# Kernel optimization log

Measured on AMD Instinct MI355X. Metric: run time of the kernel, lower is better.

## Reference

```python
import jax, jax.numpy as jnp
import numpy as np

N_NODES = 50000
N_EDGES = 625000
IN_CH = 128
OUT_CH = 128


def setup_inputs() -> dict:
    key = jax.random.key(0)
    k1, k2, k3, k4 = jax.random.split(key, 4)
    x = jax.random.normal(k1, (N_NODES, IN_CH), dtype=jnp.float32)
    edge_index = jax.random.randint(k2, (2, N_EDGES), 0, N_NODES, dtype=jnp.int64)
    # nn.Linear(in, out): weight [out, in], bias [out]
    bound = 1.0 / np.sqrt(IN_CH)
    W = jax.random.uniform(k3, (OUT_CH, IN_CH), minval=-bound, maxval=bound, dtype=jnp.float32)
    b = jax.random.uniform(k4, (OUT_CH,), minval=-bound, maxval=bound, dtype=jnp.float32)
    return {"x": x, "edge_index": edge_index, "W": W, "b": b}


def reference(x, edge_index, W, b):
    row, col = edge_index[0], edge_index[1]
    num_nodes = x.shape[0]
    # degree of destination nodes (scatter_add of ones over row)
    deg = jax.ops.segment_sum(jnp.ones(row.shape[0], dtype=x.dtype), row,
                              num_segments=num_nodes)
    deg_inv_sqrt = jnp.where(deg > 0, jax.lax.rsqrt(jnp.maximum(deg, 1.0)) * jnp.where(deg > 0, 1.0, 0.0), 0.0)
    deg_inv_sqrt = jnp.where(deg > 0, deg ** -0.5, 0.0)
    norm = deg_inv_sqrt[row] * deg_inv_sqrt[col]  # [E]
    src = x[col] * norm[:, None]                  # gather + scale, [E, C]
    out = jax.ops.segment_sum(src, row, num_segments=num_nodes)  # scatter-add
    return out @ W.T + b
```

## Files before the change

### kernel.cpp

```cpp
#include <hip/hip_runtime.h>
#include <hip/hip_bf16.h>

#define NN 50000
#define NE 625000
#define CH 128
#define RSTR 32
#define NG 196
#define GCAP 4096
#define NBIN 256
#define EPB 2442

typedef __attribute__((ext_vector_type(8))) short short8;
typedef __attribute__((ext_vector_type(4))) float floatx4;

__device__ __forceinline__ ushort f2bf(float v) {
    __hip_bfloat16 h = __float2bfloat16(v);
    return *(ushort*)&h;
}
__device__ __forceinline__ float bf2f(uint u) {
    return __uint_as_float(u << 16);
}

__global__ __launch_bounds__(256) void k_prep(const float* __restrict__ x,
                                              ushort* __restrict__ xb,
                                              const float* __restrict__ W,
                                              ushort* __restrict__ whi,
                                              ushort* __restrict__ wlo,
                                              const int* __restrict__ row,
                                              const int* __restrict__ col,
                                              uint* __restrict__ gbase,
                                              uint* __restrict__ gseg) {
    __shared__ uint h[NG];
    __shared__ uint sc[NG];
    __shared__ uint gb[NG];
    __shared__ uint cur[NG];
    __shared__ uint ss[256];
    __shared__ uint pk[EPB];

    int b = blockIdx.x;
    int t = threadIdx.x;
    if (b < NBIN) {
        int e0 = b * EPB;
        int n = NE - e0; if (n > EPB) n = EPB;

        for (int i = t; i < NG; i += 256) h[i] = 0;
        __syncthreads();

        int r[10], c[10];
#pragma unroll
        for (int j = 0; j < 10; ++j) {
            int i = t + j * 256;
            int idx = (i < n) ? (e0 + i) : e0;
            r[j] = row[idx];
            c[j] = col[idx];
        }
#pragma unroll
        for (int j = 0; j < 10; ++j)
            if (t + j * 256 < n) atomicAdd(&h[r[j] >> 8], 1u);
        __syncthreads();

        ss[t] = (t < NG) ? h[t] : 0u;
        __syncthreads();
        for (int off = 1; off < 256; off <<= 1) {
            uint add = (t >= off) ? ss[t - off] : 0u;
            __syncthreads();
            ss[t] += add;
            __syncthreads();
        }
        if (t < NG) {
            uint ex = (t == 0) ? 0u : ss[t - 1];
            sc[t] = ex;
            cur[t] = ex;
            if (h[t] > 0) gb[t] = atomicAdd(&gbase[t], h[t]);
        }
        __syncthreads();

#pragma unroll
        for (int j = 0; j < 10; ++j) {
            if (t + j * 256 < n) {
                int g = r[j] >> 8;
                uint p = atomicAdd(&cur[g], 1u);
                pk[p] = ((uint)(r[j] & 255) << 16) | (uint)(c[j] & 0xffff);
            }
        }
        __syncthreads();

        for (int i = t; i < n; i += 256) {
            int lo = 0, hi = NG - 1;
            while (lo < hi) {
                int mid = (lo + hi + 1) >> 1;
                if (sc[mid] <= (uint)i) lo = mid; else hi = mid - 1;
            }
            int g = lo;
            uint off = gb[g] + ((uint)i - sc[g]);
            if (off < GCAP) gseg[(size_t)g * GCAP + off] = pk[i];
        }
    } else if (b < 6506) {
        int i = ((b - 256) * 256 + t) * 4;
        float4 v = *(const float4*)(x + i);
        ushort4 o;
        o.x = f2bf(v.x); o.y = f2bf(v.y); o.z = f2bf(v.z); o.w = f2bf(v.w);
        *(ushort4*)(xb + i) = o;
    } else {
        int i = (b - 6506) * 256 + t;
        float v = W[i];
        ushort hh = f2bf(v);
        whi[i] = hh;
        wlo[i] = f2bf(v - bf2f((uint)hh));
    }
}

__global__ __launch_bounds__(256) void k_csr(const uint* __restrict__ gseg,
                                             const uint* __restrict__ gcnt,
                                             uint* __restrict__ csr,
                                             int* __restrict__ deg_c,
                                             float* __restrict__ nrm) {
    __shared__ ushort slots[64][62];
    __shared__ uint dcnt[64];
    int g = blockIdx.x >> 2;
    int q = blockIdx.x & 3;
    int t = threadIdx.x;

    int n = (int)gcnt[g];
    if (n > GCAP) n = GCAP;
    if (t < 64) dcnt[t] = 0;
    __syncthreads();

    const uint* seg = gseg + (size_t)g * GCAP;
    for (int i = t; i < n; i += 256) {
        uint p = seg[i];
        int rl = (int)(p >> 16);
        if ((rl >> 6) == q) {
            int r6 = rl & 63;
            uint k = atomicAdd(&dcnt[r6], 1u);
            if (k < 62) slots[r6][k] = (ushort)(p & 0xffff);
        }
    }
    __syncthreads();

    int row0 = g * 256 + q * 64;
    for (int i = t; i < 2048; i += 256) {
        int rl = i >> 5, w = i & 31;
        int rr = row0 + rl;
        if (rr < NN) {
            uint val;
            if (w == 0) val = dcnt[rl];
            else val = (uint)slots[rl][2 * w - 2] | ((uint)slots[rl][2 * w - 1] << 16);
            csr[(size_t)rr * RSTR + w] = val;
        }
    }
    if (t < 64) {
        int rr = row0 + t;
        if (rr < NN) {
            int d = (int)dcnt[t];
            deg_c[rr] = d;
            nrm[rr] = (d > 0) ? rsqrtf((float)d) : 0.0f;
        }
    }
}

__global__ __launch_bounds__(256) void k_agg(const ushort* __restrict__ xb,
                                             const int* __restrict__ deg_c,
                                             const float* __restrict__ nrm,
                                             const uint* __restrict__ csr,
                                             ushort* __restrict__ ahi) {
    const int wave = threadIdx.x >> 6;
    const int lane = threadIdx.x & 63;
    const int node = blockIdx.x * 4 + wave;
    const int deg = deg_c[node];
    const float dr = nrm[node];

    const ushort* slots = (const ushort*)(csr + node * RSTR) + 2;
    int li = (lane < 62) ? lane : 0;
    ushort craw = slots[li];
    int cli = (lane < deg) ? (int)craw : 0;
    float nl = (lane < deg) ? nrm[cli] : 0.0f;

    float ax = 0.0f, ay = 0.0f;
    for (int j = 0; j < deg; j += 8) {
#pragma unroll
        for (int u = 0; u < 8; ++u) {
            int cc = __shfl(cli, j + u);
            float nn = __shfl(nl, j + u);
            ushort2 v = ((const ushort2*)(xb + (size_t)cc * CH))[lane];
            ax = fmaf(bf2f((uint)v.x), nn, ax);
            ay = fmaf(bf2f((uint)v.y), nn, ay);
        }
    }

    ushort2 hv;
    hv.x = f2bf(ax * dr);
    hv.y = f2bf(ay * dr);
    ((ushort2*)(ahi + (size_t)node * CH))[lane] = hv;
}

__global__ __launch_bounds__(256) void k_mfma(const ushort* __restrict__ ahi,
                                              const ushort* __restrict__ whi,
                                              const ushort* __restrict__ wlo,
                                              const float* __restrict__ bias,
                                              float* __restrict__ out) {
    const int wave = threadIdx.x >> 6;
    const int lane = threadIdx.x & 63;
    const int quad = lane >> 4;
    const int r16 = lane & 15;
    const int m0 = blockIdx.x * 32;
    const int nt0 = wave * 2, nt1 = nt0 + 1;

    const ushort* a0p  = ahi + (size_t)(m0 + r16) * CH + quad * 8;
    const ushort* a1p  = a0p + 16 * CH;
    const ushort* bh0p = whi + (size_t)(nt0 * 16 + r16) * CH + quad * 8;
    const ushort* bl0p = wlo + (size_t)(nt0 * 16 + r16) * CH + quad * 8;
    const ushort* bh1p = whi + (size_t)(nt1 * 16 + r16) * CH + quad * 8;
    const ushort* bl1p = wlo + (size_t)(nt1 * 16 + r16) * CH + quad * 8;

    float b0 = bias[nt0 * 16 + r16];
    float b1 = bias[nt1 * 16 + r16];
    floatx4 acc00 = {b0, b0, b0, b0};
    floatx4 acc01 = {b1, b1, b1, b1};
    floatx4 acc10 = {b0, b0, b0, b0};
    floatx4 acc11 = {b1, b1, b1, b1};

#pragma unroll
    for (int kb = 0; kb < 4; ++kb) {
        const int k0 = kb * 32;
        short8 a0 = *(const short8*)(a0p + k0);
        short8 a1 = *(const short8*)(a1p + k0);
        short8 h0 = *(const short8*)(bh0p + k0);
        short8 l0 = *(const short8*)(bl0p + k0);
        short8 h1 = *(const short8*)(bh1p + k0);
        short8 l1 = *(const short8*)(bl1p + k0);
        acc00 = __builtin_amdgcn_mfma_f32_16x16x32_bf16(a0, h0, acc00, 0, 0, 0);
        acc00 = __builtin_amdgcn_mfma_f32_16x16x32_bf16(a0, l0, acc00, 0, 0, 0);
        acc01 = __builtin_amdgcn_mfma_f32_16x16x32_bf16(a0, h1, acc01, 0, 0, 0);
        acc01 = __builtin_amdgcn_mfma_f32_16x16x32_bf16(a0, l1, acc01, 0, 0, 0);
        acc10 = __builtin_amdgcn_mfma_f32_16x16x32_bf16(a1, h0, acc10, 0, 0, 0);
        acc10 = __builtin_amdgcn_mfma_f32_16x16x32_bf16(a1, l0, acc10, 0, 0, 0);
        acc11 = __builtin_amdgcn_mfma_f32_16x16x32_bf16(a1, h1, acc11, 0, 0, 0);
        acc11 = __builtin_amdgcn_mfma_f32_16x16x32_bf16(a1, l1, acc11, 0, 0, 0);
    }

#pragma unroll
    for (int r = 0; r < 4; ++r) {
        int row0 = m0 + quad * 4 + r;
        int row1 = row0 + 16;
        if (row0 < NN) {
            out[(size_t)row0 * CH + nt0 * 16 + r16] = acc00[r];
            out[(size_t)row0 * CH + nt1 * 16 + r16] = acc01[r];
        }
        if (row1 < NN) {
            out[(size_t)row1 * CH + nt0 * 16 + r16] = acc10[r];
            out[(size_t)row1 * CH + nt1 * 16 + r16] = acc11[r];
        }
    }
}

extern "C" void kernel_launch(void* const* d_in, const int* in_sizes, int n_in,
                              void* d_out, int out_size, void* d_ws, size_t ws_size,
                              hipStream_t stream) {
    const float* x = (const float*)d_in[0];
    const int* ei = (const int*)d_in[1];
    const float* W = (const float*)d_in[2];
    const float* b = (const float*)d_in[3];
    float* out = (float*)d_out;

    uint* csr = (uint*)d_ws;
    int* deg_c = (int*)(csr + (size_t)NN * RSTR);
    float* nrm = (float*)(deg_c + 50176);
    ushort* ahi = (ushort*)(nrm + 50176);
    ushort* xb = ahi + (size_t)(NN + 16) * CH;
    ushort* whi = xb + (size_t)NN * CH;
    ushort* wlo = whi + CH * CH;
    uint* gbase = (uint*)(wlo + CH * CH);
    uint* gseg = gbase + 256;

    hipMemsetAsync(gbase, 0, NG * sizeof(uint), stream);
    k_prep<<<6570, 256, 0, stream>>>(x, xb, W, whi, wlo, ei, ei + NE, gbase, gseg);
    k_csr<<<NG * 4, 256, 0, stream>>>(gseg, gbase, csr, deg_c, nrm);
    k_agg<<<NN / 4, 256, 0, stream>>>(xb, deg_c, nrm, csr, ahi);
    k_mfma<<<(NN + 31) / 32, 256, 0, stream>>>(ahi, whi, wlo, b, out);
}
```

Baseline: 145.5 us.

## Fuse neighbor aggregation into MFMA GEMM kernel via swizzled LDS tile

Merges the aggregation and linear-transform kernels into one. Each block aggregates 32 nodes (8 per wave) into a swizzled bf16 LDS tile and then runs the MFMA GEMM from LDS, so the intermediate aggregated matrix no longer makes a global-memory round trip and one launch is dropped. The gather now has each half-wave fetch a different neighbor with 8-byte loads, combined by a cross-half shuffle. Next-node metadata is prefetched while the current node is processed. The cost is fewer, heavier blocks (one per 32 nodes instead of one per 4), which may reduce latency hiding in the gather phase.

```diff
diff --git a/kernel.cpp b/kernel.cpp
--- a/kernel.cpp
+++ b/kernel.cpp
@@ -159,55 +159,82 @@
     }
 }
 
-__global__ __launch_bounds__(256) void k_agg(const ushort* __restrict__ xb,
-                                             const int* __restrict__ deg_c,
-                                             const float* __restrict__ nrm,
-                                             const uint* __restrict__ csr,
-                                             ushort* __restrict__ ahi) {
-    const int wave = threadIdx.x >> 6;
-    const int lane = threadIdx.x & 63;
-    const int node = blockIdx.x * 4 + wave;
-    const int deg = deg_c[node];
-    const float dr = nrm[node];
-
-    const ushort* slots = (const ushort*)(csr + node * RSTR) + 2;
-    int li = (lane < 62) ? lane : 0;
-    ushort craw = slots[li];
-    int cli = (lane < deg) ? (int)craw : 0;
-    float nl = (lane < deg) ? nrm[cli] : 0.0f;
-
-    float ax = 0.0f, ay = 0.0f;
-    for (int j = 0; j < deg; j += 8) {
-#pragma unroll
-        for (int u = 0; u < 8; ++u) {
-            int cc = __shfl(cli, j + u);
-            float nn = __shfl(nl, j + u);
-            ushort2 v = ((const ushort2*)(xb + (size_t)cc * CH))[lane];
-            ax = fmaf(bf2f((uint)v.x), nn, ax);
-            ay = fmaf(bf2f((uint)v.y), nn, ay);
-        }
-    }
-
-    ushort2 hv;
-    hv.x = f2bf(ax * dr);
-    hv.y = f2bf(ay * dr);
-    ((ushort2*)(ahi + (size_t)node * CH))[lane] = hv;
-}
-
-__global__ __launch_bounds__(256) void k_mfma(const ushort* __restrict__ ahi,
+__global__ __launch_bounds__(256) void k_aggm(const ushort* __restrict__ xb,
+                                              const int* __restrict__ deg_c,
+                                              const float* __restrict__ nrm,
+                                              const uint* __restrict__ csr,
                                               const ushort* __restrict__ whi,
                                               const ushort* __restrict__ wlo,
                                               const float* __restrict__ bias,
                                               float* __restrict__ out) {
+    __shared__ ushort at[32 * 128];
     const int wave = threadIdx.x >> 6;
     const int lane = threadIdx.x & 63;
+    const int half = lane >> 5;
+    const int lq = lane & 31;
+    const int m0 = blockIdx.x * 32;
+    const int li = (lane < 62) ? lane : 0;
+
+    int node0 = m0 + wave * 8;
+    int deg_n = 0; ushort craw_n = 0; float dr_n = 0.0f;
+    if (node0 < NN) {
+        deg_n  = deg_c[node0];
+        craw_n = ((const ushort*)(csr + (size_t)node0 * RSTR))[2 + li];
+        dr_n   = nrm[node0];
+    }
+    for (int s = 0; s < 8; ++s) {
+        int node = node0 + s;
+        int r = wave * 8 + s;
+        if (node >= NN) {
+            if (half == 0) {
+                int byte = (r * 256 + lq * 8) ^ ((r & 7) << 4);
+                *(uint2*)((char*)at + byte) = make_uint2(0u, 0u);
+            }
+            continue;
+        }
+        int deg = deg_n; ushort craw = craw_n; float dr = dr_n;
+        int cli = (lane < deg) ? (int)craw : 0;
+        float nl = (lane < deg) ? nrm[cli] : 0.0f;
+        int nxt = node + 1;
+        if (s < 7 && nxt < NN) {
+            deg_n  = deg_c[nxt];
+            craw_n = ((const ushort*)(csr + (size_t)nxt * RSTR))[2 + li];
+            dr_n   = nrm[nxt];
+        }
+        float a0 = 0.f, a1 = 0.f, a2 = 0.f, a3 = 0.f;
+        for (int j = 0; j < deg; j += 8) {
+#pragma unroll
+            for (int up = 0; up < 4; ++up) {
+                int i0 = j + 2 * up;
+                int   c0 = __builtin_amdgcn_readlane(cli, i0);
+                int   c1 = __builtin_amdgcn_readlane(cli, i0 + 1);
+                float n0 = __uint_as_float(__builtin_amdgcn_readlane(__float_as_uint(nl), i0));
+                float n1 = __uint_as_float(__builtin_amdgcn_readlane(__float_as_uint(nl), i0 + 1));
+                int   cc = half ? c1 : c0;
+                float nw = half ? n1 : n0;
+                uint2 v = *(const uint2*)(xb + (size_t)cc * CH + lq * 4);
+                a0 = fmaf(__uint_as_float(v.x << 16),          nw, a0);
+                a1 = fmaf(__uint_as_float(v.x & 0xffff0000u),  nw, a1);
+                a2 = fmaf(__uint_as_float(v.y << 16),          nw, a2);
+                a3 = fmaf(__uint_as_float(v.y & 0xffff0000u),  nw, a3);
+            }
+        }
+        a0 += __shfl_xor(a0, 32);
+        a1 += __shfl_xor(a1, 32);
+        a2 += __shfl_xor(a2, 32);
+        a3 += __shfl_xor(a3, 32);
+        if (half == 0) {
+            uint w0 = (uint)f2bf(a0 * dr) | ((uint)f2bf(a1 * dr) << 16);
+            uint w1 = (uint)f2bf(a2 * dr) | ((uint)f2bf(a3 * dr) << 16);
+            int byte = (r * 256 + lq * 8) ^ ((r & 7) << 4);
+            *(uint2*)((char*)at + byte) = make_uint2(w0, w1);
+        }
+    }
+    __syncthreads();
+
     const int quad = lane >> 4;
     const int r16 = lane & 15;
-    const int m0 = blockIdx.x * 32;
     const int nt0 = wave * 2, nt1 = nt0 + 1;
-
-    const ushort* a0p  = ahi + (size_t)(m0 + r16) * CH + quad * 8;
-    const ushort* a1p  = a0p + 16 * CH;
     const ushort* bh0p = whi + (size_t)(nt0 * 16 + r16) * CH + quad * 8;
     const ushort* bl0p = wlo + (size_t)(nt0 * 16 + r16) * CH + quad * 8;
     const ushort* bh1p = whi + (size_t)(nt1 * 16 + r16) * CH + quad * 8;
@@ -220,23 +247,25 @@
     floatx4 acc10 = {b0, b0, b0, b0};
     floatx4 acc11 = {b1, b1, b1, b1};
 
+    const int swz = (r16 & 7) << 4;
 #pragma unroll
     for (int kb = 0; kb < 4; ++kb) {
+        const int cb = quad * 16 + kb * 64;
+        short8 A0 = *(const short8*)((const char*)at + ((r16 * 256 + cb) ^ swz));
+        short8 A1 = *(const short8*)((const char*)at + (((r16 + 16) * 256 + cb) ^ swz));
         const int k0 = kb * 32;
-        short8 a0 = *(const short8*)(a0p + k0);
-        short8 a1 = *(const short8*)(a1p + k0);
         short8 h0 = *(const short8*)(bh0p + k0);
         short8 l0 = *(const short8*)(bl0p + k0);
         short8 h1 = *(const short8*)(bh1p + k0);
         short8 l1 = *(const short8*)(bl1p + k0);
-        acc00 = __builtin_amdgcn_mfma_f32_16x16x32_bf16(a0, h0, acc00, 0, 0, 0);
-        acc00 = __builtin_amdgcn_mfma_f32_16x16x32_bf16(a0, l0, acc00, 0, 0, 0);
-        acc01 = __builtin_amdgcn_mfma_f32_16x16x32_bf16(a0, h1, acc01, 0, 0, 0);
-        acc01 = __builtin_amdgcn_mfma_f32_16x16x32_bf16(a0, l1, acc01, 0, 0, 0);
-        acc10 = __builtin_amdgcn_mfma_f32_16x16x32_bf16(a1, h0, acc10, 0, 0, 0);
-        acc10 = __builtin_amdgcn_mfma_f32_16x16x32_bf16(a1, l0, acc10, 0, 0, 0);
-        acc11 = __builtin_amdgcn_mfma_f32_16x16x32_bf16(a1, h1, acc11, 0, 0, 0);
-        acc11 = __builtin_amdgcn_mfma_f32_16x16x32_bf16(a1, l1, acc11, 0, 0, 0);
+        acc00 = __builtin_amdgcn_mfma_f32_16x16x32_bf16(A0, h0, acc00, 0, 0, 0);
+        acc00 = __builtin_amdgcn_mfma_f32_16x16x32_bf16(A0, l0, acc00, 0, 0, 0);
+        acc01 = __builtin_amdgcn_mfma_f32_16x16x32_bf16(A0, h1, acc01, 0, 0, 0);
+        acc01 = __builtin_amdgcn_mfma_f32_16x16x32_bf16(A0, l1, acc01, 0, 0, 0);
+        acc10 = __builtin_amdgcn_mfma_f32_16x16x32_bf16(A1, h0, acc10, 0, 0, 0);
+        acc10 = __builtin_amdgcn_mfma_f32_16x16x32_bf16(A1, l0, acc10, 0, 0, 0);
+        acc11 = __builtin_amdgcn_mfma_f32_16x16x32_bf16(A1, h1, acc11, 0, 0, 0);
+        acc11 = __builtin_amdgcn_mfma_f32_16x16x32_bf16(A1, l1, acc11, 0, 0, 0);
     }
 
 #pragma unroll
@@ -276,6 +305,5 @@
     hipMemsetAsync(gbase, 0, NG * sizeof(uint), stream);
     k_prep<<<6570, 256, 0, stream>>>(x, xb, W, whi, wlo, ei, ei + NE, gbase, gseg);
     k_csr<<<NG * 4, 256, 0, stream>>>(gseg, gbase, csr, deg_c, nrm);
-    k_agg<<<NN / 4, 256, 0, stream>>>(xb, deg_c, nrm, csr, ahi);
-    k_mfma<<<(NN + 31) / 32, 256, 0, stream>>>(ahi, whi, wlo, b, out);
-}
+    k_aggm<<<(NN + 31) / 32, 256, 0, stream>>>(xb, deg_c, nrm, csr, whi, wlo, b, out);
+}
```

Result: faster. 141.1 us (-3.0%).
